# Kernel optimization log

Measured on AMD Instinct MI355X. Metric: run time of the kernel, lower is better.

The kernel has to match this reference:

```python
import jax, jax.numpy as jnp
import numpy as np

VOCAB, D, H = 32000, 1024, 16
DH = D // H
DFF = 4 * D
EPS = 1e-5


def layer_norm(x, g, b):
    mu = jnp.mean(x, axis=-1, keepdims=True)
    var = jnp.var(x, axis=-1, keepdims=True)
    return (x - mu) * jax.lax.rsqrt(var + EPS) * g + b


def pos_enc(seq_len, d_model):
    # faithful to the torch double-loop: angle = pos / 10000**(2*i/d) for even index i
    pos = jnp.arange(seq_len, dtype=jnp.float32)[:, None]          # [S,1]
    i_even = jnp.arange(0, d_model, 2, dtype=jnp.float32)[None, :]  # [1,D/2]
    angle = pos / jnp.power(10000.0, 2.0 * i_even / d_model)        # [S,D/2]
    pe = jnp.zeros((seq_len, d_model), dtype=jnp.float32)
    pe = pe.at[:, 0::2].set(jnp.sin(angle))
    pe = pe.at[:, 1::2].set(jnp.cos(angle))
    return pe


def setup_inputs() -> dict:
    key = jax.random.key(0)
    ks = jax.random.split(key, 16)
    s = 0.02
    return {
        "tokens": jax.random.randint(ks[0], (4, 2048), 0, VOCAB),
        "emb": jax.random.normal(ks[1], (VOCAB, D), jnp.float32) * s,
        "in_proj_w": jax.random.normal(ks[2], (3 * D, D), jnp.float32) * s,
        "in_proj_b": jnp.zeros((3 * D,), jnp.float32),
        "out_proj_w": jax.random.normal(ks[3], (D, D), jnp.float32) * s,
        "out_proj_b": jnp.zeros((D,), jnp.float32),
        "w1": jax.random.normal(ks[4], (DFF, D), jnp.float32) * s,
        "b1": jnp.zeros((DFF,), jnp.float32),
        "w2": jax.random.normal(ks[5], (D, DFF), jnp.float32) * s,
        "b2": jnp.zeros((D,), jnp.float32),
        "g1": jnp.ones((D,), jnp.float32),
        "beta1": jnp.zeros((D,), jnp.float32),
        "g2": jnp.ones((D,), jnp.float32),
        "beta2": jnp.zeros((D,), jnp.float32),
    }


def reference(tokens, emb, in_proj_w, in_proj_b, out_proj_w, out_proj_b,
              w1, b1, w2, b2, g1, beta1, g2, beta2):
    B, S = tokens.shape
    x = emb[tokens] + pos_enc(S, D)[None, :, :]                 # [B,S,D]
    # multi-head self-attention (eval mode, no dropout)
    qkv = x @ in_proj_w.T + in_proj_b                           # [B,S,3D]
    q, k, v = jnp.split(qkv, 3, axis=-1)
    q = q.reshape(B, S, H, DH)
    k = k.reshape(B, S, H, DH)
    v = v.reshape(B, S, H, DH)
    scores = jnp.einsum("bqhd,bkhd->bhqk", q, k) / jnp.sqrt(jnp.float32(DH))
    attn = jax.nn.softmax(scores, axis=-1)
    ctx = jnp.einsum("bhqk,bkhd->bqhd", attn, v).reshape(B, S, D)
    attn_out = ctx @ out_proj_w.T + out_proj_b
    h = layer_norm(x + attn_out, g1, beta1)
    ff = jax.nn.relu(h @ w1.T + b1) @ w2.T + b2
    return layer_norm(h + ff, g2, beta2)
```

## Files before the change

### kernel.cpp

```cpp
#include <hip/hip_runtime.h>
#include <math.h>

#define DMODEL 1024
#define NH 16
#define DHEAD 64
#define DFF 4096
#define BATCH 4
#define SEQ 2048
#define MROWS (BATCH * SEQ)
#define LNEPS 1e-5f
#define NT (SEQ / 64)

typedef __attribute__((ext_vector_type(8))) short bf16x8;
typedef __attribute__((ext_vector_type(4))) float f32x4;
typedef __attribute__((ext_vector_type(16))) float f32x16;
typedef __attribute__((ext_vector_type(4))) unsigned int u32x4;

__device__ inline unsigned short f2bf(float f) {
  unsigned int u = __float_as_uint(f);
  unsigned int r = (u + 0x7fffu + ((u >> 16) & 1u)) >> 16;
  return (unsigned short)r;
}
__device__ inline float bf2f(unsigned short b) {
  return __uint_as_float(((unsigned int)b) << 16);
}

__device__ inline void gload16(const unsigned short* g, char* l) {
  __builtin_amdgcn_global_load_lds(
      (const __attribute__((address_space(1))) unsigned int*)g,
      (__attribute__((address_space(3))) unsigned int*)l, 16, 0, 0);
}

__device__ inline float fexp2(float x) {
  float r;
  asm("v_exp_f32 %0, %1" : "=v"(r) : "v"(x));
  return r;
}
__device__ inline unsigned int cvtpk(float lo, float hi) {
  unsigned int r;
  asm("v_cvt_pk_bf16_f32 %0, %1, %2" : "=v"(r) : "v"(lo), "v"(hi));
  return r;
}
__device__ inline void plswap(unsigned int& a, unsigned int& b) {
  asm("v_permlane32_swap_b32 %0, %1" : "+v"(a), "+v"(b));
}

__global__ __launch_bounds__(256)
void embed_kernel(const int* __restrict__ tokens, const float* __restrict__ emb,
                  unsigned short* __restrict__ Xb) {
  const int HALF = DMODEL / 2;
  int idx = blockIdx.x * 256 + threadIdx.x;
  if (idx >= MROWS * HALF) return;
  int row = idx / HALF;
  int j = idx - row * HALF;
  int s = row & (SEQ - 1);
  int tok = tokens[row];
  float2 e = ((const float2*)(emb + (size_t)tok * DMODEL))[j];
  float denom = powf(10000.0f, (2.0f * (float)(2 * j)) / (float)DMODEL);
  float ang = (float)s / denom;
  float sn, cs;
  sincosf(ang, &sn, &cs);
  ushort2 ob;
  ob.x = f2bf(e.x + sn);
  ob.y = f2bf(e.y + cs);
  ((ushort2*)(Xb + (size_t)row * DMODEL))[j] = ob;
}

__global__ __launch_bounds__(256)
void cvt4_kernel(const float* __restrict__ a, const float* __restrict__ b,
                 const float* __restrict__ c, const float* __restrict__ d,
                 unsigned short* __restrict__ oa, unsigned short* __restrict__ ob,
                 unsigned short* __restrict__ oc, unsigned short* __restrict__ od) {
  int i = blockIdx.x * 256 + threadIdx.x;
  const float* src; unsigned short* dst; int off;
  if (i < 786432)       { src = a; dst = oa; off = 0; }
  else if (i < 1048576) { src = b; dst = ob; off = 786432; }
  else if (i < 2097152) { src = c; dst = oc; off = 1048576; }
  else                  { src = d; dst = od; off = 2097152; }
  int j = i - off;
  float4 v = ((const float4*)src)[j];
  ushort4 o;
  o.x = f2bf(v.x); o.y = f2bf(v.y); o.z = f2bf(v.z); o.w = f2bf(v.w);
  ((ushort4*)dst)[j] = o;
}

__device__ inline void sthalf8(const unsigned short* G, int grow0, int K, int kt,
                               char* smem_, int isB, int half, int t) {
  char* dst = smem_ + ((kt & 1) * 65536) + isB * 32768 + half * 16384;
#pragma unroll
  for (int i = 0; i < 2; ++i) {
    int g = i * 512 + t;
    int r = g >> 3, sl = g & 7;
    int c = sl ^ (r & 7);
    gload16(G + (size_t)(grow0 + half * 128 + r) * K + kt * 64 + c * 8, dst + g * 16);
  }
}

#define VM4_ asm volatile("s_waitcnt vmcnt(4)" ::: "memory")
#define VM2_ asm volatile("s_waitcnt vmcnt(2)" ::: "memory")
#define VM0_ asm volatile("s_waitcnt vmcnt(0)" ::: "memory")

#define PHASE8(bufofs, MG, NP, LA, LB, STAGE_STMT, WAIT_STMT)                   \
  {                                                                             \
    if (LA) {                                                                   \
      _Pragma("unroll") for (int m = 0; m < 4; ++m) {                           \
        int arow = wm * 128 + (MG) * 64 + m * 16 + fr;                          \
        _Pragma("unroll") for (int ks = 0; ks < 2; ++ks)                        \
          af[m][ks] = *(const bf16x8*)(smem + (bufofs) + arow * 128 +           \
                        (((ks * 4 + fq) ^ (arow & 7)) * 16));                   \
      }                                                                         \
    }                                                                           \
    if (LB) {                                                                   \
      _Pragma("unroll") for (int nn = 0; nn < 2; ++nn) {                        \
        int n = (NP) * 2 + nn;                                                  \
        int brow = wn * 64 + n * 16 + fr;                                       \
        _Pragma("unroll") for (int ks = 0; ks < 2; ++ks)                        \
          bf[(NP) * 2 + nn][ks] = *(const bf16x8*)(smem + (bufofs) + 32768 +    \
                        brow * 128 + (((ks * 4 + fq) ^ (brow & 7)) * 16));      \
      }                                                                         \
    }                                                                           \
    STAGE_STMT;                                                                 \
    __builtin_amdgcn_sched_barrier(0);                                          \
    __builtin_amdgcn_s_barrier();                                               \
    asm volatile("s_waitcnt lgkmcnt(0)" ::: "memory");                          \
    __builtin_amdgcn_sched_barrier(0);                                          \
    __builtin_amdgcn_s_setprio(1);                                              \
    _Pragma("unroll") for (int m = 0; m < 4; ++m)                               \
      _Pragma("unroll") for (int nn = 0; nn < 2; ++nn)                          \
        _Pragma("unroll") for (int ks = 0; ks < 2; ++ks)                        \
          acc[(MG) * 4 + m][(NP) * 2 + nn] =                                    \
              __builtin_amdgcn_mfma_f32_16x16x32_bf16(                          \
                  af[m][ks], bf[(NP) * 2 + nn][ks],                             \
                  acc[(MG) * 4 + m][(NP) * 2 + nn], 0, 0, 0);                   \
    __builtin_amdgcn_s_setprio(0);                                              \
    WAIT_STMT;                                                                  \
    __builtin_amdgcn_sched_barrier(0);                                          \
    __builtin_amdgcn_s_barrier();                                               \
    __builtin_amdgcn_sched_barrier(0);                                          \
  }

__global__ __launch_bounds__(512, 2)
void gemm8p(const unsigned short* __restrict__ A, const unsigned short* __restrict__ B,
            const float* __restrict__ bias, const float* __restrict__ resid,
            float* __restrict__ Cf, unsigned short* __restrict__ Cb,
            int M, int N, int K, int relu) {
  extern __shared__ char smem[];

  const int t = threadIdx.x;
  const int lane = t & 63;
  const int wv = t >> 6;
  const int wm = wv >> 2;
  const int wn = wv & 3;
  const int fr = lane & 15;
  const int fq = lane >> 4;

  const int nwg = gridDim.x;
  const int orig = blockIdx.x;
  const int q8 = nwg >> 3;
  const int wgid = (orig & 7) * q8 + (orig >> 3);
  const int stid = wgid >> 2, within = wgid & 3;
  const int sm = within & 1, sn = within >> 1;
  const int Msup = M >> 9;
  const int stm = stid % Msup, stn = stid / Msup;
  const int m0 = (stm * 2 + sm) * 256;
  const int n0 = (stn * 2 + sn) * 256;

  f32x4 acc[8][4];
#pragma unroll
  for (int m = 0; m < 8; ++m)
#pragma unroll
    for (int n = 0; n < 4; ++n) acc[m][n] = (f32x4){0.f, 0.f, 0.f, 0.f};

  const int nk = K / 64;
  const int nj = nk / 2;

  sthalf8(A, m0, K, 0, smem, 0, 0, t);
  sthalf8(A, m0, K, 0, smem, 0, 1, t);
  sthalf8(B, n0, K, 0, smem, 1, 0, t);
  sthalf8(B, n0, K, 0, smem, 1, 1, t);
  sthalf8(B, n0, K, 1, smem, 1, 0, t);
  sthalf8(B, n0, K, 1, smem, 1, 1, t);
  VM4_;
  __builtin_amdgcn_sched_barrier(0);
  __builtin_amdgcn_s_barrier();
  __builtin_amdgcn_sched_barrier(0);

  bf16x8 af[4][2];
  bf16x8 bf[4][2];

  for (int j = 0; j < nj; ++j) {
    const bool st = (j + 1 < nj);
    PHASE8(0, 0, 0, 1, 1, sthalf8(A, m0, K, 2 * j + 1, smem, 0, 0, t), );
    PHASE8(0, 0, 1, 0, 1, sthalf8(A, m0, K, 2 * j + 1, smem, 0, 1, t), );
    PHASE8(0, 1, 1, 1, 0,
           if (st) sthalf8(B, n0, K, 2 * j + 2, smem, 1, 0, t), );
    PHASE8(0, 1, 0, 0, 0,
           if (st) sthalf8(B, n0, K, 2 * j + 2, smem, 1, 1, t),
           { if (st) { VM4_; } else { VM0_; } });
    PHASE8(65536, 0, 0, 1, 1,
           if (st) sthalf8(A, m0, K, 2 * j + 2, smem, 0, 0, t), );
    PHASE8(65536, 0, 1, 0, 1,
           if (st) sthalf8(A, m0, K, 2 * j + 2, smem, 0, 1, t), );
    PHASE8(65536, 1, 1, 1, 0,
           if (st) sthalf8(B, n0, K, 2 * j + 3, smem, 1, 0, t), );
    PHASE8(65536, 1, 0, 0, 0,
           if (st) sthalf8(B, n0, K, 2 * j + 3, smem, 1, 1, t),
           { if (st) { VM4_; } });
  }

  float* slab = (float*)(smem + wv * 4352);
#pragma unroll
  for (int m = 0; m < 8; ++m) {
#pragma unroll
    for (int n = 0; n < 4; ++n)
#pragma unroll
      for (int j = 0; j < 4; ++j)
        slab[(fq * 4 + j) * 68 + n * 16 + fr] = acc[m][n][j];
    int rg0 = m0 + wm * 128 + m * 16;
#pragma unroll
    for (int it = 0; it < 4; ++it) {
      int u = it * 64 + lane;
      int row = u >> 4, seg = u & 15;
      float4 v = *(const float4*)&slab[row * 68 + seg * 4];
      int col = n0 + wn * 64 + seg * 4;
      float4 b4 = *(const float4*)&bias[col];
      v.x += b4.x; v.y += b4.y; v.z += b4.z; v.w += b4.w;
      if (relu) {
        v.x = fmaxf(v.x, 0.f); v.y = fmaxf(v.y, 0.f);
        v.z = fmaxf(v.z, 0.f); v.w = fmaxf(v.w, 0.f);
      }
      size_t idx = (size_t)(rg0 + row) * N + col;
      if (resid) {
        float4 r4 = *(const float4*)&resid[idx];
        v.x += r4.x; v.y += r4.y; v.z += r4.z; v.w += r4.w;
      }
      if (Cf) {
        *(float4*)&Cf[idx] = v;
      } else {
        ushort4 ob;
        ob.x = f2bf(v.x); ob.y = f2bf(v.y); ob.z = f2bf(v.z); ob.w = f2bf(v.w);
        *(ushort4*)&Cb[idx] = ob;
      }
    }
  }
}

__device__ inline void stA128(const unsigned short* G, int m0, int K, int kt,
                              int half, char* smem_, int t) {
  char* dst = smem_ + ((kt & 1) * 49152) + half * 16384;
#pragma unroll
  for (int i = 0; i < 2; ++i) {
    int g = i * 512 + t;
    int r = g >> 3, sl = g & 7;
    int c = sl ^ (r & 7);
    gload16(G + (size_t)(m0 + half * 128 + r) * K + kt * 64 + c * 8, dst + g * 16);
  }
}
__device__ inline void stB128(const unsigned short* G, int n0, int K, int kt,
                              char* smem_, int t) {
  char* dst = smem_ + ((kt & 1) * 49152) + 32768;
#pragma unroll
  for (int i = 0; i < 2; ++i) {
    int g = i * 512 + t;
    int r = g >> 3, sl = g & 7;
    int c = sl ^ (r & 7);
    gload16(G + (size_t)(n0 + r) * K + kt * 64 + c * 8, dst + g * 16);
  }
}

#define PH128(bufofs, MG, NP, LA, LB, STAGE_STMT, WAIT_STMT)                    \
  {                                                                             \
    if (LA) {                                                                   \
      _Pragma("unroll") for (int mm = 0; mm < 2; ++mm) {                        \
        int arow = wm * 64 + ((MG) * 2 + mm) * 16 + fr;                         \
        _Pragma("unroll") for (int ks = 0; ks < 2; ++ks)                        \
          af[mm][ks] = *(const bf16x8*)(smem + (bufofs) + arow * 128 +          \
                        (((ks * 4 + fq) ^ (arow & 7)) * 16));                   \
      }                                                                         \
    }                                                                           \
    if (LB) {                                                                   \
      _Pragma("unroll") for (int nn = 0; nn < 2; ++nn) {                        \
        int n = (NP) * 2 + nn;                                                  \
        int brow = wn * 64 + n * 16 + fr;                                       \
        _Pragma("unroll") for (int ks = 0; ks < 2; ++ks)                        \
          bf[(NP) * 2 + nn][ks] = *(const bf16x8*)(smem + (bufofs) + 32768 +    \
                        brow * 128 + (((ks * 4 + fq) ^ (brow & 7)) * 16));      \
      }                                                                         \
    }                                                                           \
    STAGE_STMT;                                                                 \
    __builtin_amdgcn_sched_barrier(0);                                          \
    __builtin_amdgcn_s_barrier();                                               \
    asm volatile("s_waitcnt lgkmcnt(0)" ::: "memory");                          \
    __builtin_amdgcn_sched_barrier(0);                                          \
    __builtin_amdgcn_s_setprio(1);                                              \
    _Pragma("unroll") for (int mm = 0; mm < 2; ++mm)                            \
      _Pragma("unroll") for (int nn = 0; nn < 2; ++nn)                          \
        _Pragma("unroll") for (int ks = 0; ks < 2; ++ks)                        \
          acc[(MG) * 2 + mm][(NP) * 2 + nn] =                                   \
              __builtin_amdgcn_mfma_f32_16x16x32_bf16(                          \
                  af[mm][ks], bf[(NP) * 2 + nn][ks],                            \
                  acc[(MG) * 2 + mm][(NP) * 2 + nn], 0, 0, 0);                  \
    __builtin_amdgcn_s_setprio(0);                                              \
    WAIT_STMT;                                                                  \
    __builtin_amdgcn_sched_barrier(0);                                          \
    __builtin_amdgcn_s_barrier();                                               \
    __builtin_amdgcn_sched_barrier(0);                                          \
  }

__global__ __launch_bounds__(512, 2)
void gemm8p128(const unsigned short* __restrict__ A, const unsigned short* __restrict__ B,
               const float* __restrict__ bias, const float* __restrict__ resid,
               const unsigned short* __restrict__ residb,
               float* __restrict__ Cf, unsigned short* __restrict__ Cb,
               int M, int N, int K, int relu) {
  extern __shared__ char smem[];

  const int t = threadIdx.x;
  const int lane = t & 63;
  const int wv = t >> 6;
  const int wm = wv >> 1;
  const int wn = wv & 1;
  const int fr = lane & 15;
  const int fq = lane >> 4;

  const int nwg = gridDim.x;
  const int orig = blockIdx.x;
  const int q8 = nwg >> 3;
  const int wgid = (orig & 7) * q8 + (orig >> 3);
  const int stid = wgid >> 2, within = wgid & 3;
  const int sm = within & 1, sn = within >> 1;
  const int Msup = M >> 9;
  const int stm = stid % Msup, stn = stid / Msup;
  const int m0 = (stm * 2 + sm) * 256;
  const int n0 = (stn * 2 + sn) * 128;

  f32x4 acc[4][4];
#pragma unroll
  for (int m = 0; m < 4; ++m)
#pragma unroll
    for (int n = 0; n < 4; ++n) acc[m][n] = (f32x4){0.f, 0.f, 0.f, 0.f};

  const int nk = K / 64;
  const int nj = nk / 2;

  stA128(A, m0, K, 0, 0, smem, t);
  stA128(A, m0, K, 0, 1, smem, t);
  stB128(B, n0, K, 0, smem, t);
  stB128(B, n0, K, 1, smem, t);
  VM2_;
  __builtin_amdgcn_sched_barrier(0);
  __builtin_amdgcn_s_barrier();
  __builtin_amdgcn_sched_barrier(0);

  bf16x8 af[2][2];
  bf16x8 bf[4][2];

  for (int j = 0; j < nj; ++j) {
    const bool st = (j + 1 < nj);
    const int k1 = 2 * j + 1;
    PH128(0, 0, 0, 1, 1, stA128(A, m0, K, k1, 0, smem, t), );
    PH128(0, 0, 1, 0, 1, stA128(A, m0, K, k1, 1, smem, t), );
    PH128(0, 1, 0, 1, 0,
          if (st) stB128(B, n0, K, k1 + 1, smem, t), );
    PH128(0, 1, 1, 0, 0,
          if (st) stA128(A, m0, K, k1 + 1, 0, smem, t),
          { if (st) { VM4_; } else { VM0_; } });
    PH128(49152, 0, 0, 1, 1,
          if (st) stA128(A, m0, K, k1 + 1, 1, smem, t), );
    PH128(49152, 0, 1, 0, 1, , );
    PH128(49152, 1, 0, 1, 0,
          if (st) stB128(B, n0, K, k1 + 2, smem, t), );
    PH128(49152, 1, 1, 0, 0, ,
          { if (st) { VM2_; } });
  }

  float* slab = (float*)(smem + wv * 4352);
#pragma unroll
  for (int m = 0; m < 4; ++m) {
#pragma unroll
    for (int n = 0; n < 4; ++n)
#pragma unroll
      for (int j = 0; j < 4; ++j)
        slab[(fq * 4 + j) * 68 + n * 16 + fr] = acc[m][n][j];
    int rg0 = m0 + wm * 64 + m * 16;
#pragma unroll
    for (int it = 0; it < 4; ++it) {
      int u = it * 64 + lane;
      int row = u >> 4, seg = u & 15;
      float4 v = *(const float4*)&slab[row * 68 + seg * 4];
      int col = n0 + wn * 64 + seg * 4;
      float4 b4 = *(const float4*)&bias[col];
      v.x += b4.x; v.y += b4.y; v.z += b4.z; v.w += b4.w;
      if (relu) {
        v.x = fmaxf(v.x, 0.f); v.y = fmaxf(v.y, 0.f);
        v.z = fmaxf(v.z, 0.f); v.w = fmaxf(v.w, 0.f);
      }
      size_t idx = (size_t)(rg0 + row) * N + col;
      if (resid) {
        float4 r4 = *(const float4*)&resid[idx];
        v.x += r4.x; v.y += r4.y; v.z += r4.z; v.w += r4.w;
      } else if (residb) {
        ushort4 r4 = *(const ushort4*)&residb[idx];
        v.x += bf2f(r4.x); v.y += bf2f(r4.y); v.z += bf2f(r4.z); v.w += bf2f(r4.w);
      }
      if (Cf) {
        *(float4*)&Cf[idx] = v;
      } else {
        ushort4 ob;
        ob.x = f2bf(v.x); ob.y = f2bf(v.y); ob.z = f2bf(v.z); ob.w = f2bf(v.w);
        *(ushort4*)&Cb[idx] = ob;
      }
    }
  }
}

__global__ __launch_bounds__(256)
void vtrans_kernel(const unsigned short* __restrict__ qkvb, unsigned short* __restrict__ vtb) {
  __shared__ __align__(16) unsigned short tile[64][64];
  const int st = blockIdx.x;
  const int bh = blockIdx.y;
  const int b = bh >> 4, h = bh & 15;
  const int t = threadIdx.x;
#pragma unroll
  for (int p = 0; p < 2; ++p) {
    int item = p * 256 + t;
    int r = item >> 3, c8 = item & 7;
    const unsigned short* src =
        qkvb + (size_t)(b * SEQ + st * 64 + r) * (3 * DMODEL) + 2048 + h * 64 + c8 * 8;
    *(uint4*)&tile[r][(c8 ^ (r & 7)) * 8] = *(const uint4*)src;
  }
  __syncthreads();
#pragma unroll
  for (int p = 0; p < 2; ++p) {
    int item = p * 256 + t;
    int d = item & 63, s8 = item >> 6;
    unsigned short v[8];
#pragma unroll
    for (int e = 0; e < 8; ++e) {
      int s = s8 * 8 + e;
      v[e] = tile[s][(((d >> 3) ^ (s & 7)) * 8) + (d & 7)];
    }
    uint4 u;
    u.x = (unsigned int)v[0] | ((unsigned int)v[1] << 16);
    u.y = (unsigned int)v[2] | ((unsigned int)v[3] << 16);
    u.z = (unsigned int)v[4] | ((unsigned int)v[5] << 16);
    u.w = (unsigned int)v[6] | ((unsigned int)v[7] << 16);
    *(uint4*)(vtb + ((size_t)bh * 64 + d) * SEQ + st * 64 + s8 * 8) = u;
  }
}

__global__ __launch_bounds__(512, 4)
void attn_kernel(const unsigned short* __restrict__ qkv, const unsigned short* __restrict__ vtb,
                 unsigned short* __restrict__ ctxb) {
  __shared__ __align__(16) unsigned short Ks[2][64][64];
  __shared__ __align__(16) unsigned short Vts[2][64][64];
  __shared__ __align__(16) unsigned short Slab[8][32][64];

  const int t = threadIdx.x;
  const int lane = t & 63;
  const int wq = t >> 6;
  const int l31 = lane & 31;
  const int hi1 = lane >> 5;
  const int bid = blockIdx.x;
  const int bh = bid & 63;
  const int qt = bid >> 6;
  const int b = bh >> 4, h = bh & 15;
  const int q0 = qt * 256;

  const size_t RS = 3 * DMODEL;
  const unsigned short* qb = qkv + (size_t)b * SEQ * RS + h * DHEAD;
  const unsigned short* kb = qb + DMODEL;

  bf16x8 qf[4];
  {
    const unsigned short* qrow = qb + (size_t)(q0 + wq * 32 + l31) * RS;
#pragma unroll
    for (int s = 0; s < 4; ++s)
      qf[s] = *(const bf16x8*)(qrow + s * 16 + hi1 * 8);
  }

  const unsigned short* kgl =
      kb + (size_t)(wq * 8 + (lane >> 3)) * RS + ((lane & 7) ^ (lane >> 3)) * 8;
  const unsigned short* vgl =
      vtb + ((size_t)bh * 64 + wq * 8 + (lane >> 3)) * SEQ + ((lane & 7) ^ (lane >> 3)) * 8;

  f32x16 oacc[2] = {};
  float lacc = 0.f;

  gload16(kgl, (char*)&Ks[0][wq * 8][0]);
  gload16(vgl, (char*)&Vts[0][wq * 8][0]);
  __syncthreads();

  const float C = 0.18033688011112042f;

  for (int kt = 0; kt < NT; ++kt) {
    const int cur = kt & 1;
    if (kt + 1 < NT) {
      gload16(kgl + (size_t)(kt + 1) * 64 * RS, (char*)&Ks[cur ^ 1][wq * 8][0]);
      gload16(vgl + (size_t)(kt + 1) * 64, (char*)&Vts[cur ^ 1][wq * 8][0]);
    }

    f32x16 sacc[2] = {};
    __builtin_amdgcn_s_setprio(1);
#pragma unroll
    for (int s = 0; s < 4; ++s) {
#pragma unroll
      for (int kvt = 0; kvt < 2; ++kvt) {
        int row = kvt * 32 + l31;
        bf16x8 kf = *(const bf16x8*)&Ks[cur][row][(((2 * s + hi1) ^ (row & 7)) * 8)];
        sacc[kvt] = __builtin_amdgcn_mfma_f32_32x32x16_bf16(kf, qf[s], sacc[kvt], 0, 0, 0);
      }
    }
    __builtin_amdgcn_s_setprio(0);

#pragma unroll
    for (int kvt = 0; kvt < 2; ++kvt) {
      float p[16];
#pragma unroll
      for (int r = 0; r < 16; ++r) p[r] = fexp2(sacc[kvt][r] * C);
      float ps = 0.f;
#pragma unroll
      for (int r = 0; r < 16; ++r) ps += p[r];
      lacc += ps;
#pragma unroll
      for (int half = 0; half < 2; ++half) {
        const int lo = half * 8;
        unsigned int x0 = cvtpk(p[lo + 0], p[lo + 1]);
        unsigned int x1 = cvtpk(p[lo + 2], p[lo + 3]);
        unsigned int y0 = cvtpk(p[lo + 4], p[lo + 5]);
        unsigned int y1 = cvtpk(p[lo + 6], p[lo + 7]);
        plswap(x0, y0);
        plswap(x1, y1);
        bf16x8 pa = __builtin_bit_cast(bf16x8, (u32x4){x0, x1, y0, y1});
        const int s2 = kvt * 2 + half;
        __builtin_amdgcn_s_setprio(1);
#pragma unroll
        for (int dt = 0; dt < 2; ++dt) {
          int vrow = dt * 32 + l31;
          bf16x8 vf = *(const bf16x8*)&Vts[cur][vrow][(((2 * s2 + hi1) ^ (vrow & 7)) * 8)];
          oacc[dt] = __builtin_amdgcn_mfma_f32_32x32x16_bf16(pa, vf, oacc[dt], 0, 0, 0);
        }
        __builtin_amdgcn_s_setprio(0);
      }
    }
    __syncthreads();
  }

  lacc += __shfl_xor(lacc, 32);
  float inv = 1.0f / lacc;

  float iv[16];
#pragma unroll
  for (int r = 0; r < 16; ++r)
    iv[r] = __shfl(inv, (r & 3) + 8 * (r >> 2) + 4 * hi1);

#pragma unroll
  for (int dt = 0; dt < 2; ++dt) {
    const int chunk = dt * 4 + (l31 >> 3);
    const int e7 = l31 & 7;
#pragma unroll
    for (int r = 0; r < 16; ++r) {
      int qp = (r & 3) + 8 * (r >> 2) + 4 * hi1;
      Slab[wq][qp][((chunk ^ (qp & 7)) * 8) + e7] = f2bf(oacc[dt][r] * iv[r]);
    }
  }
#pragma unroll
  for (int it = 0; it < 4; ++it) {
    int u = it * 64 + lane;
    int row = u >> 3, s = u & 7;
    uint4 v = *(const uint4*)&Slab[wq][row][((s ^ (row & 7)) * 8)];
    *(uint4*)(ctxb + (size_t)(b * SEQ + q0 + wq * 32 + row) * DMODEL + h * DHEAD + s * 8) = v;
  }
}

__global__ __launch_bounds__(256)
void ln_kernel(const float* __restrict__ Zf, const unsigned short* __restrict__ Zb,
               const float* __restrict__ g, const float* __restrict__ bta,
               float* __restrict__ Yf, unsigned short* __restrict__ Yb) {
  const int row = blockIdx.x;
  float4 v;
  if (Zf) {
    v = ((const float4*)(Zf + (size_t)row * DMODEL))[threadIdx.x];
  } else {
    ushort4 u = ((const ushort4*)(Zb + (size_t)row * DMODEL))[threadIdx.x];
    v.x = bf2f(u.x); v.y = bf2f(u.y); v.z = bf2f(u.z); v.w = bf2f(u.w);
  }
  float s = v.x + v.y + v.z + v.w;
  float ss = fmaf(v.x, v.x, fmaf(v.y, v.y, fmaf(v.z, v.z, v.w * v.w)));
#pragma unroll
  for (int o = 32; o >= 1; o >>= 1) {
    s += __shfl_xor(s, o);
    ss += __shfl_xor(ss, o);
  }
  __shared__ float red[8];
  int w = threadIdx.x >> 6;
  if ((threadIdx.x & 63) == 0) { red[w] = s; red[4 + w] = ss; }
  __syncthreads();
  s = red[0] + red[1] + red[2] + red[3];
  ss = red[4] + red[5] + red[6] + red[7];
  float mu = s * (1.0f / DMODEL);
  float var = ss * (1.0f / DMODEL) - mu * mu;
  float rs = rsqrtf(var + LNEPS);
  float4 gg = ((const float4*)g)[threadIdx.x];
  float4 bb = ((const float4*)bta)[threadIdx.x];
  float4 o;
  o.x = (v.x - mu) * rs * gg.x + bb.x;
  o.y = (v.y - mu) * rs * gg.y + bb.y;
  o.z = (v.z - mu) * rs * gg.z + bb.z;
  o.w = (v.w - mu) * rs * gg.w + bb.w;
  if (Yf) ((float4*)(Yf + (size_t)row * DMODEL))[threadIdx.x] = o;
  if (Yb) {
    ushort4 ob;
    ob.x = f2bf(o.x); ob.y = f2bf(o.y); ob.z = f2bf(o.z); ob.w = f2bf(o.w);
    ((ushort4*)(Yb + (size_t)row * DMODEL))[threadIdx.x] = ob;
  }
}

extern "C" void kernel_launch(void* const* d_in, const int* in_sizes, int n_in,
                              void* d_out, int out_size, void* d_ws, size_t ws_size,
                              hipStream_t stream) {
  const int* tokens       = (const int*)d_in[0];
  const float* emb        = (const float*)d_in[1];
  const float* in_proj_w  = (const float*)d_in[2];
  const float* in_proj_b  = (const float*)d_in[3];
  const float* out_proj_w = (const float*)d_in[4];
  const float* out_proj_b = (const float*)d_in[5];
  const float* w1         = (const float*)d_in[6];
  const float* b1         = (const float*)d_in[7];
  const float* w2         = (const float*)d_in[8];
  const float* b2         = (const float*)d_in[9];
  const float* g1         = (const float*)d_in[10];
  const float* beta1      = (const float*)d_in[11];
  const float* g2         = (const float*)d_in[12];
  const float* beta2      = (const float*)d_in[13];
  float* out = (float*)d_out;

  char* ws = (char*)d_ws;
  const size_t MB = 1ull << 20;
  unsigned short* inwb  = (unsigned short*)(ws + 0 * MB);
  unsigned short* outwb = (unsigned short*)(ws + 6 * MB);
  unsigned short* w1b   = (unsigned short*)(ws + 8 * MB);
  unsigned short* w2b   = (unsigned short*)(ws + 16 * MB);
  float* y2             = (float*)(ws + 24 * MB);
  unsigned short* xb    = (unsigned short*)(ws + 56 * MB);
  unsigned short* qkvb  = (unsigned short*)(ws + 72 * MB);
  unsigned short* hpre_b = (unsigned short*)(ws + 72 * MB);
  unsigned short* hb    = (unsigned short*)(ws + 104 * MB);
  unsigned short* vtb   = (unsigned short*)(ws + 120 * MB);
  unsigned short* ctxb  = (unsigned short*)(ws + 136 * MB);
  unsigned short* ffbb  = (unsigned short*)(ws + 120 * MB);

  const size_t GLDSP  = 131072;
  const size_t GLDSPN = 98304;

  embed_kernel<<<(MROWS * (DMODEL / 2) + 255) / 256, 256, 0, stream>>>(tokens, emb, xb);
  cvt4_kernel<<<12288, 256, 0, stream>>>(in_proj_w, out_proj_w, w1, w2,
                                         inwb, outwb, w1b, w2b);
  gemm8p<<<(MROWS / 256) * (3 * DMODEL / 256), 512, GLDSP, stream>>>(
      xb, inwb, in_proj_b, nullptr, nullptr, qkvb, MROWS, 3 * DMODEL, DMODEL, 0);
  vtrans_kernel<<<dim3(SEQ / 64, BATCH * NH), 256, 0, stream>>>(qkvb, vtb);
  attn_kernel<<<(SEQ / 256) * (BATCH * NH), 512, 0, stream>>>(qkvb, vtb, ctxb);
  gemm8p128<<<(MROWS / 256) * (DMODEL / 128), 512, GLDSPN, stream>>>(
      ctxb, outwb, out_proj_b, nullptr, xb, nullptr, hpre_b, MROWS, DMODEL, DMODEL, 0);
  ln_kernel<<<MROWS, 256, 0, stream>>>(nullptr, hpre_b, g1, beta1, nullptr, hb);
  gemm8p<<<(MROWS / 256) * (DFF / 256), 512, GLDSP, stream>>>(
      hb, w1b, b1, nullptr, nullptr, ffbb, MROWS, DFF, DMODEL, 1);
  gemm8p128<<<(MROWS / 256) * (DMODEL / 128), 512, GLDSPN, stream>>>(
      ffbb, w2b, b2, nullptr, hb, y2, nullptr, MROWS, DMODEL, DFF, 0);
  ln_kernel<<<MROWS, 256, 0, stream>>>(y2, nullptr, g2, beta2, out, nullptr);
}
```

Baseline: 391.7 us.

## Merge prep kernels, use narrow-tile GEMM for QKV, store FFN output in bf16

Fuses the embedding and weight-conversion kernels into one launch to save a kernel launch. Switches the QKV projection from the 256-wide-N GEMM to the 128-wide-N variant, which doubles the block count and uses less LDS per block. Writes the second FFN GEMM result as bf16 instead of fp32 before the final layer norm, halving that intermediate's traffic at some cost in precision.

Result: no change. 385.2 us (-1.6%).

```diff
diff --git a/kernel.cpp b/kernel.cpp
--- a/kernel.cpp
+++ b/kernel.cpp
@@ -46,42 +46,42 @@
 }
 
 __global__ __launch_bounds__(256)
-void embed_kernel(const int* __restrict__ tokens, const float* __restrict__ emb,
-                  unsigned short* __restrict__ Xb) {
-  const int HALF = DMODEL / 2;
-  int idx = blockIdx.x * 256 + threadIdx.x;
-  if (idx >= MROWS * HALF) return;
-  int row = idx / HALF;
-  int j = idx - row * HALF;
-  int s = row & (SEQ - 1);
-  int tok = tokens[row];
-  float2 e = ((const float2*)(emb + (size_t)tok * DMODEL))[j];
-  float denom = powf(10000.0f, (2.0f * (float)(2 * j)) / (float)DMODEL);
-  float ang = (float)s / denom;
-  float sn, cs;
-  sincosf(ang, &sn, &cs);
-  ushort2 ob;
-  ob.x = f2bf(e.x + sn);
-  ob.y = f2bf(e.y + cs);
-  ((ushort2*)(Xb + (size_t)row * DMODEL))[j] = ob;
-}
-
-__global__ __launch_bounds__(256)
-void cvt4_kernel(const float* __restrict__ a, const float* __restrict__ b,
+void prep_kernel(const int* __restrict__ tokens, const float* __restrict__ emb,
+                 unsigned short* __restrict__ Xb,
+                 const float* __restrict__ a, const float* __restrict__ b,
                  const float* __restrict__ c, const float* __restrict__ d,
                  unsigned short* __restrict__ oa, unsigned short* __restrict__ ob,
                  unsigned short* __restrict__ oc, unsigned short* __restrict__ od) {
-  int i = blockIdx.x * 256 + threadIdx.x;
-  const float* src; unsigned short* dst; int off;
-  if (i < 786432)       { src = a; dst = oa; off = 0; }
-  else if (i < 1048576) { src = b; dst = ob; off = 786432; }
-  else if (i < 2097152) { src = c; dst = oc; off = 1048576; }
-  else                  { src = d; dst = od; off = 2097152; }
-  int j = i - off;
-  float4 v = ((const float4*)src)[j];
-  ushort4 o;
-  o.x = f2bf(v.x); o.y = f2bf(v.y); o.z = f2bf(v.z); o.w = f2bf(v.w);
-  ((ushort4*)dst)[j] = o;
+  const int bid = blockIdx.x;
+  if (bid < 16384) {
+    const int HALF = DMODEL / 2;
+    int idx = bid * 256 + threadIdx.x;
+    int row = idx / HALF;
+    int j = idx - row * HALF;
+    int s = row & (SEQ - 1);
+    int tok = tokens[row];
+    float2 e = ((const float2*)(emb + (size_t)tok * DMODEL))[j];
+    float denom = powf(10000.0f, (2.0f * (float)(2 * j)) / (float)DMODEL);
+    float ang = (float)s / denom;
+    float sn, cs;
+    sincosf(ang, &sn, &cs);
+    ushort2 o2;
+    o2.x = f2bf(e.x + sn);
+    o2.y = f2bf(e.y + cs);
+    ((ushort2*)(Xb + (size_t)row * DMODEL))[j] = o2;
+  } else {
+    int i = (bid - 16384) * 256 + threadIdx.x;
+    const float* src; unsigned short* dst; int off;
+    if (i < 786432)       { src = a; dst = oa; off = 0; }
+    else if (i < 1048576) { src = b; dst = ob; off = 786432; }
+    else if (i < 2097152) { src = c; dst = oc; off = 1048576; }
+    else                  { src = d; dst = od; off = 2097152; }
+    int j = i - off;
+    float4 v = ((const float4*)src)[j];
+    ushort4 o;
+    o.x = f2bf(v.x); o.y = f2bf(v.y); o.z = f2bf(v.z); o.w = f2bf(v.w);
+    ((ushort4*)dst)[j] = o;
+  }
 }
 
 __device__ inline void sthalf8(const unsigned short* G, int grow0, int K, int kt,
@@ -637,27 +637,27 @@
 
   char* ws = (char*)d_ws;
   const size_t MB = 1ull << 20;
-  unsigned short* inwb  = (unsigned short*)(ws + 0 * MB);
-  unsigned short* outwb = (unsigned short*)(ws + 6 * MB);
-  unsigned short* w1b   = (unsigned short*)(ws + 8 * MB);
-  unsigned short* w2b   = (unsigned short*)(ws + 16 * MB);
-  float* y2             = (float*)(ws + 24 * MB);
-  unsigned short* xb    = (unsigned short*)(ws + 56 * MB);
-  unsigned short* qkvb  = (unsigned short*)(ws + 72 * MB);
+  unsigned short* inwb   = (unsigned short*)(ws + 0 * MB);
+  unsigned short* outwb  = (unsigned short*)(ws + 6 * MB);
+  unsigned short* w1b    = (unsigned short*)(ws + 8 * MB);
+  unsigned short* w2b    = (unsigned short*)(ws + 16 * MB);
+  unsigned short* y2b    = (unsigned short*)(ws + 24 * MB);
+  unsigned short* xb     = (unsigned short*)(ws + 56 * MB);
+  unsigned short* qkvb   = (unsigned short*)(ws + 72 * MB);
   unsigned short* hpre_b = (unsigned short*)(ws + 72 * MB);
-  unsigned short* hb    = (unsigned short*)(ws + 104 * MB);
-  unsigned short* vtb   = (unsigned short*)(ws + 120 * MB);
-  unsigned short* ctxb  = (unsigned short*)(ws + 136 * MB);
-  unsigned short* ffbb  = (unsigned short*)(ws + 120 * MB);
+  unsigned short* hb     = (unsigned short*)(ws + 104 * MB);
+  unsigned short* vtb    = (unsigned short*)(ws + 120 * MB);
+  unsigned short* ctxb   = (unsigned short*)(ws + 136 * MB);
+  unsigned short* ffbb   = (unsigned short*)(ws + 120 * MB);
 
   const size_t GLDSP  = 131072;
   const size_t GLDSPN = 98304;
 
-  embed_kernel<<<(MROWS * (DMODEL / 2) + 255) / 256, 256, 0, stream>>>(tokens, emb, xb);
-  cvt4_kernel<<<12288, 256, 0, stream>>>(in_proj_w, out_proj_w, w1, w2,
+  prep_kernel<<<28672, 256, 0, stream>>>(tokens, emb, xb,
+                                         in_proj_w, out_proj_w, w1, w2,
                                          inwb, outwb, w1b, w2b);
-  gemm8p<<<(MROWS / 256) * (3 * DMODEL / 256), 512, GLDSP, stream>>>(
-      xb, inwb, in_proj_b, nullptr, nullptr, qkvb, MROWS, 3 * DMODEL, DMODEL, 0);
+  gemm8p128<<<(MROWS / 256) * (3 * DMODEL / 128), 512, GLDSPN, stream>>>(
+      xb, inwb, in_proj_b, nullptr, nullptr, nullptr, qkvb, MROWS, 3 * DMODEL, DMODEL, 0);
   vtrans_kernel<<<dim3(SEQ / 64, BATCH * NH), 256, 0, stream>>>(qkvb, vtb);
   attn_kernel<<<(SEQ / 256) * (BATCH * NH), 512, 0, stream>>>(qkvb, vtb, ctxb);
   gemm8p128<<<(MROWS / 256) * (DMODEL / 128), 512, GLDSPN, stream>>>(
@@ -666,6 +666,6 @@
   gemm8p<<<(MROWS / 256) * (DFF / 256), 512, GLDSP, stream>>>(
       hb, w1b, b1, nullptr, nullptr, ffbb, MROWS, DFF, DMODEL, 1);
   gemm8p128<<<(MROWS / 256) * (DMODEL / 128), 512, GLDSPN, stream>>>(
-      ffbb, w2b, b2, nullptr, hb, y2, nullptr, MROWS, DMODEL, DFF, 0);
-  ln_kernel<<<MROWS, 256, 0, stream>>>(y2, nullptr, g2, beta2, out, nullptr);
-}
+      ffbb, w2b, b2, nullptr, hb, nullptr, y2b, MROWS, DMODEL, DFF, 0);
+  ln_kernel<<<MROWS, 256, 0, stream>>>(nullptr, y2b, g2, beta2, out, nullptr);
+}
```
